# Kernel tuning notes

Hardware: AMD Instinct MI355X
Metric: run time of the kernel (lower is better)

Reference implementation:

```python
import jax, jax.numpy as jnp
import numpy as np
import math

N_EMBD = 1024
N_HEAD = 16
BLOCK = 2048
B, T = 2, 2048


def setup_inputs() -> dict:
    key = jax.random.key(0)
    ks = jax.random.split(key, 5)
    s = 0.02
    return {
        "x": jax.random.normal(ks[0], (B, T, N_EMBD), dtype=jnp.float32),
        "W_attn": jax.random.normal(ks[1], (3 * N_EMBD, N_EMBD), dtype=jnp.float32) * s,  # [out,in] torch layout
        "b_attn": jax.random.normal(ks[2], (3 * N_EMBD,), dtype=jnp.float32) * s,
        "W_proj": jax.random.normal(ks[3], (N_EMBD, N_EMBD), dtype=jnp.float32) * s,
        "b_proj": jax.random.normal(ks[4], (N_EMBD,), dtype=jnp.float32) * s,
    }


def reference(x, W_attn, b_attn, W_proj, b_proj):
    Bx, Tx, C = x.shape
    H = N_HEAD
    D = C // H
    qkv = jnp.einsum("btc,oc->bto", x, W_attn) + b_attn  # [B,T,3C]
    q, k, v = jnp.split(qkv, 3, axis=-1)
    # [B,T,H,D] -> [B,H,T,D]
    q = q.reshape(Bx, Tx, H, D).transpose(0, 2, 1, 3)
    k = k.reshape(Bx, Tx, H, D).transpose(0, 2, 1, 3)
    v = v.reshape(Bx, Tx, H, D).transpose(0, 2, 1, 3)
    att = jnp.einsum("bhqd,bhkd->bhqk", q, k) * (1.0 / math.sqrt(D))
    causal = jnp.tril(jnp.ones((Tx, Tx), dtype=bool))
    att = jnp.where(causal[None, None], att, -jnp.inf)
    att = jax.nn.softmax(att, axis=-1)
    y = jnp.einsum("bhqk,bhkd->bhqd", att, v)  # [B,H,T,D]
    y = y.transpose(0, 2, 1, 3).reshape(Bx, Tx, C)
    y = jnp.einsum("btc,oc->bto", y, W_proj) + b_proj
    return y
```

## Files before the change

### kernel.cpp

```cpp
#include <hip/hip_runtime.h>
#include <hip/hip_bf16.h>
#include <stdint.h>

typedef unsigned short u16;
using f32x4 = __attribute__((ext_vector_type(4))) float;
using s16x8 = __attribute__((ext_vector_type(8))) short;

#define B_SZ 2
#define T_SZ 2048
#define C_SZ 1024
#define H_SZ 16
#define D_SZ 64

__device__ __forceinline__ u16 f2bf(float f) {
  union { float f; uint32_t u; } c; c.f = f;
  uint32_t u = c.u;
  u += 0x7FFFu + ((u >> 16) & 1u);
  return (u16)(u >> 16);
}

__device__ __forceinline__ void async16(const u16* g, u16* l) {
  __builtin_amdgcn_global_load_lds((__attribute__((address_space(1))) void*)(g),
                                   (__attribute__((address_space(3))) void*)(l),
                                   16, 0, 0);
}

__global__ void cvt3_kernel(const float* __restrict__ a, int na,
                            const float* __restrict__ b, int nb,
                            const float* __restrict__ c, int nc,
                            u16* __restrict__ out) {
  int n = na + nb + nc;
  for (int i = blockIdx.x * blockDim.x + threadIdx.x; i < n; i += gridDim.x * blockDim.x) {
    const float* src; int off;
    if (i < na)           { src = a; off = i; }
    else if (i < na + nb) { src = b; off = i - na; }
    else                  { src = c; off = i - na - nb; }
    float4 v = reinterpret_cast<const float4*>(src)[off];
    ushort4 o;
    o.x = f2bf(v.x); o.y = f2bf(v.y); o.z = f2bf(v.z); o.w = f2bf(v.w);
    reinterpret_cast<ushort4*>(out)[i] = o;
  }
}

__global__ __launch_bounds__(256) void gemm_qkv(
    const u16* __restrict__ A, const u16* __restrict__ W,
    const float* __restrict__ bias,
    u16* __restrict__ Qo, u16* __restrict__ Ko, u16* __restrict__ Vt)
{
  const int K = 1024;
  const int NT = 32;
  __shared__ __align__(16) u16 lA[2][128 * 32];
  __shared__ __align__(16) u16 lB[2][128 * 32];
  int tid = threadIdx.x, lane = tid & 63, wave = tid >> 6;
  int wm = (wave >> 1) * 64, wn = (wave & 1) * 64;
  int bm = blockIdx.x * 128, bn = blockIdx.y * 128;
  int r = lane & 15, g = lane >> 4;

  int p0 = tid, p1 = 256 + tid;
  int ar0 = p0 >> 2, ar1 = p1 >> 2;
  int al0 = (p0 & 3) ^ (ar0 & 3), al1 = (p1 & 3) ^ (ar1 & 3);
  const u16* As0 = A + (size_t)(bm + ar0) * K + al0 * 8;
  const u16* As1 = A + (size_t)(bm + ar1) * K + al1 * 8;
  const u16* Ws0 = W + (size_t)(bn + ar0) * K + al0 * 8;
  const u16* Ws1 = W + (size_t)(bn + ar1) * K + al1 * 8;

  f32x4 acc[4][4];
#pragma unroll
  for (int i = 0; i < 4; ++i)
#pragma unroll
    for (int j = 0; j < 4; ++j)
      acc[i][j] = (f32x4){0.f, 0.f, 0.f, 0.f};

  int rd_off = r * 32 + ((g ^ (r & 3)) * 8);

  async16(As0, &lA[0][p0 * 8]);
  async16(As1, &lA[0][p1 * 8]);
  async16(Ws0, &lB[0][p0 * 8]);
  async16(Ws1, &lB[0][p1 * 8]);
  __syncthreads();

  int cur = 0;
  for (int t = 0; t < NT; ++t) {
    if (t + 1 < NT) {
      int k0 = (t + 1) * 32;
      int nb_ = cur ^ 1;
      async16(As0 + k0, &lA[nb_][p0 * 8]);
      async16(As1 + k0, &lA[nb_][p1 * 8]);
      async16(Ws0 + k0, &lB[nb_][p0 * 8]);
      async16(Ws1 + k0, &lB[nb_][p1 * 8]);
    }
    s16x8 af[4], bf[4];
#pragma unroll
    for (int i = 0; i < 4; ++i)
      af[i] = *(const s16x8*)(&lA[cur][(wm + i * 16) * 32 + rd_off]);
#pragma unroll
    for (int j = 0; j < 4; ++j)
      bf[j] = *(const s16x8*)(&lB[cur][(wn + j * 16) * 32 + rd_off]);
#pragma unroll
    for (int i = 0; i < 4; ++i)
#pragma unroll
      for (int j = 0; j < 4; ++j)
        acc[i][j] = __builtin_amdgcn_mfma_f32_16x16x32_bf16(af[i], bf[j], acc[i][j], 0, 0, 0);
    __syncthreads();
    cur ^= 1;
  }

  int seg = bn >> 10;
#pragma unroll
  for (int i = 0; i < 4; ++i) {
#pragma unroll
    for (int j = 0; j < 4; ++j) {
      int col = bn + wn + j * 16 + r;
      int cc = col & 1023;
      int h = cc >> 6, d = cc & 63;
      float bv = bias[col];
      int row0 = bm + wm + i * 16 + g * 4;
      int b = row0 >> 11, t0 = row0 & 2047;
      if (seg == 2) {
        ushort4 pv;
        pv.x = f2bf(acc[i][j][0] + bv);
        pv.y = f2bf(acc[i][j][1] + bv);
        pv.z = f2bf(acc[i][j][2] + bv);
        pv.w = f2bf(acc[i][j][3] + bv);
        *reinterpret_cast<ushort4*>(Vt + ((size_t)(b * H_SZ + h) * D_SZ + d) * T_SZ + t0) = pv;
      } else {
        u16* dst = (seg == 0) ? Qo : Ko;
        float scale = (seg == 0) ? 0.125f : 1.0f;
#pragma unroll
        for (int rr = 0; rr < 4; ++rr) {
          float v = (acc[i][j][rr] + bv) * scale;
          dst[(((size_t)(b * H_SZ + h) * T_SZ + (t0 + rr)) * D_SZ) + d] = f2bf(v);
        }
      }
    }
  }
}

__global__ __launch_bounds__(256) void gemm_proj(
    const u16* __restrict__ A, const u16* __restrict__ W,
    const float* __restrict__ bias, float* __restrict__ out)
{
  const int K = 1024;
  const int NT = 32;
  __shared__ __align__(16) u16 lA[2][128 * 32];
  __shared__ __align__(16) u16 lB[2][128 * 32];
  int tid = threadIdx.x, lane = tid & 63, wave = tid >> 6;
  int wm = (wave >> 1) * 64, wn = (wave & 1) * 64;
  int bm = blockIdx.x * 128, bn = blockIdx.y * 128;
  int r = lane & 15, g = lane >> 4;

  int p0 = tid, p1 = 256 + tid;
  int ar0 = p0 >> 2, ar1 = p1 >> 2;
  int al0 = (p0 & 3) ^ (ar0 & 3), al1 = (p1 & 3) ^ (ar1 & 3);
  const u16* As0 = A + (size_t)(bm + ar0) * K + al0 * 8;
  const u16* As1 = A + (size_t)(bm + ar1) * K + al1 * 8;
  const u16* Ws0 = W + (size_t)(bn + ar0) * K + al0 * 8;
  const u16* Ws1 = W + (size_t)(bn + ar1) * K + al1 * 8;

  f32x4 acc[4][4];
#pragma unroll
  for (int i = 0; i < 4; ++i)
#pragma unroll
    for (int j = 0; j < 4; ++j)
      acc[i][j] = (f32x4){0.f, 0.f, 0.f, 0.f};

  int rd_off = r * 32 + ((g ^ (r & 3)) * 8);

  async16(As0, &lA[0][p0 * 8]);
  async16(As1, &lA[0][p1 * 8]);
  async16(Ws0, &lB[0][p0 * 8]);
  async16(Ws1, &lB[0][p1 * 8]);
  __syncthreads();

  int cur = 0;
  for (int t = 0; t < NT; ++t) {
    if (t + 1 < NT) {
      int k0 = (t + 1) * 32;
      int nb_ = cur ^ 1;
      async16(As0 + k0, &lA[nb_][p0 * 8]);
      async16(As1 + k0, &lA[nb_][p1 * 8]);
      async16(Ws0 + k0, &lB[nb_][p0 * 8]);
      async16(Ws1 + k0, &lB[nb_][p1 * 8]);
    }
    s16x8 af[4], bf[4];
#pragma unroll
    for (int i = 0; i < 4; ++i)
      af[i] = *(const s16x8*)(&lA[cur][(wm + i * 16) * 32 + rd_off]);
#pragma unroll
    for (int j = 0; j < 4; ++j)
      bf[j] = *(const s16x8*)(&lB[cur][(wn + j * 16) * 32 + rd_off]);
#pragma unroll
    for (int i = 0; i < 4; ++i)
#pragma unroll
      for (int j = 0; j < 4; ++j)
        acc[i][j] = __builtin_amdgcn_mfma_f32_16x16x32_bf16(af[i], bf[j], acc[i][j], 0, 0, 0);
    __syncthreads();
    cur ^= 1;
  }

#pragma unroll
  for (int i = 0; i < 4; ++i) {
#pragma unroll
    for (int j = 0; j < 4; ++j) {
      int col = bn + wn + j * 16 + r;
      float bv = bias[col];
#pragma unroll
      for (int rr = 0; rr < 4; ++rr) {
        int row = bm + wm + i * 16 + g * 4 + rr;
        out[(size_t)row * 1024 + col] = acc[i][j][rr] + bv;
      }
    }
  }
}

__global__ __launch_bounds__(256) void attn_kernel(
    const u16* __restrict__ Q, const u16* __restrict__ K, const u16* __restrict__ Vt,
    u16* __restrict__ Y)
{
  __shared__ __align__(16) u16 lK[2][64 * 64];
  __shared__ __align__(16) u16 lV[2][64 * 64];
  __shared__ __align__(16) u16 lP[4][16 * 64];
  int tid = threadIdx.x, lane = tid & 63, wave = tid >> 6;
  int bh = blockIdx.x;
  int qt = 31 - blockIdx.y;
  const u16* Qh = Q + (size_t)bh * T_SZ * D_SZ;
  const u16* Kh = K + (size_t)bh * T_SZ * D_SZ;
  const u16* Vh = Vt + (size_t)bh * D_SZ * T_SZ;
  int r = lane & 15, g = lane >> 4;
  int wq = qt * 64 + wave * 16;
  int qrow = wq + r;

  s16x8 qf0 = *(const s16x8*)(Qh + (size_t)qrow * 64 + g * 8);
  s16x8 qf1 = *(const s16x8*)(Qh + (size_t)qrow * 64 + 32 + g * 8);

  int p0 = tid, p1 = 256 + tid;
  int r0 = p0 >> 3, r1 = p1 >> 3;
  int l0 = (p0 & 7) ^ (r0 & 7), l1 = (p1 & 7) ^ (r1 & 7);

  float m = -3e30f, s = 0.f;
  f32x4 o[4];
#pragma unroll
  for (int j = 0; j < 4; ++j) o[j] = (f32x4){0.f, 0.f, 0.f, 0.f};

  u16* lPw = lP[wave];

  async16(Kh + (size_t)r0 * 64 + l0 * 8, &lK[0][p0 * 8]);
  async16(Kh + (size_t)r1 * 64 + l1 * 8, &lK[0][p1 * 8]);
  async16(Vh + (size_t)r0 * T_SZ + l0 * 8, &lV[0][p0 * 8]);
  async16(Vh + (size_t)r1 * T_SZ + l1 * 8, &lV[0][p1 * 8]);
  __syncthreads();

  int cur = 0;
  for (int kt = 0; kt <= qt; ++kt) {
    int kvbase = kt * 64;
    if (kt < qt) {
      int nb_ = cur ^ 1;
      int kb = kvbase + 64;
      async16(Kh + (size_t)(kb + r0) * 64 + l0 * 8, &lK[nb_][p0 * 8]);
      async16(Kh + (size_t)(kb + r1) * 64 + l1 * 8, &lK[nb_][p1 * 8]);
      async16(Vh + (size_t)r0 * T_SZ + kb + l0 * 8, &lV[nb_][p0 * 8]);
      async16(Vh + (size_t)r1 * T_SZ + kb + l1 * 8, &lV[nb_][p1 * 8]);
    }

    f32x4 sf[4];
#pragma unroll
    for (int jj = 0; jj < 4; ++jj) {
      int krow = jj * 16 + r;
      const s16x8 kf0 = *(const s16x8*)(&lK[cur][krow * 64 + ((g ^ (r & 7)) * 8)]);
      const s16x8 kf1 = *(const s16x8*)(&lK[cur][krow * 64 + (((4 + g) ^ (r & 7)) * 8)]);
      f32x4 sv = (f32x4){0.f, 0.f, 0.f, 0.f};
      sv = __builtin_amdgcn_mfma_f32_16x16x32_bf16(kf0, qf0, sv, 0, 0, 0);
      sv = __builtin_amdgcn_mfma_f32_16x16x32_bf16(kf1, qf1, sv, 0, 0, 0);
      sf[jj] = sv;
    }

    float mx = -3e30f;
    if (kt == qt) {
#pragma unroll
      for (int jj = 0; jj < 4; ++jj)
#pragma unroll
        for (int rr = 0; rr < 4; ++rr) {
          int kv = kvbase + jj * 16 + g * 4 + rr;
          float v = (kv <= qrow) ? sf[jj][rr] : -3e30f;
          sf[jj][rr] = v;
          mx = fmaxf(mx, v);
        }
    } else {
#pragma unroll
      for (int jj = 0; jj < 4; ++jj)
#pragma unroll
        for (int rr = 0; rr < 4; ++rr) mx = fmaxf(mx, sf[jj][rr]);
    }
    mx = fmaxf(mx, __shfl_xor(mx, 16));
    mx = fmaxf(mx, __shfl_xor(mx, 32));

    float mnew = fmaxf(m, mx);
    float corr = __expf(m - mnew);
    m = mnew;

    float rsum = 0.f;
#pragma unroll
    for (int jj = 0; jj < 4; ++jj)
#pragma unroll
      for (int rr = 0; rr < 4; ++rr) {
        float p = __expf(sf[jj][rr] - m);
        sf[jj][rr] = p;
        rsum += p;
      }
    rsum += __shfl_xor(rsum, 16);
    rsum += __shfl_xor(rsum, 32);
    s = s * corr + rsum;

    float crr[4];
#pragma unroll
    for (int rr = 0; rr < 4; ++rr)
      crr[rr] = __shfl(corr, (lane & 48) | (g * 4 + rr), 64);
#pragma unroll
    for (int j = 0; j < 4; ++j)
#pragma unroll
      for (int rr = 0; rr < 4; ++rr) o[j][rr] *= crr[rr];

#pragma unroll
    for (int jj = 0; jj < 4; ++jj) {
      ushort4 pk;
      pk.x = f2bf(sf[jj][0]); pk.y = f2bf(sf[jj][1]);
      pk.z = f2bf(sf[jj][2]); pk.w = f2bf(sf[jj][3]);
      int off = r * 64 + ((jj * 16 + 4 * g) ^ ((r & 7) << 3));
      *reinterpret_cast<ushort4*>(lPw + off) = pk;
    }

#pragma unroll
    for (int hh = 0; hh < 2; ++hh) {
      const s16x8 pa = *(const s16x8*)(lPw + r * 64 + (((hh * 4 + g) ^ (r & 7)) * 8));
#pragma unroll
      for (int j = 0; j < 4; ++j) {
        int vrow = j * 16 + r;
        const s16x8 vb = *(const s16x8*)(&lV[cur][vrow * 64 + (((hh * 4 + g) ^ (r & 7)) * 8)]);
        o[j] = __builtin_amdgcn_mfma_f32_16x16x32_bf16(pa, vb, o[j], 0, 0, 0);
      }
    }
    __syncthreads();
    cur ^= 1;
  }

  float sinv = 1.0f / s;
  float srr[4];
#pragma unroll
  for (int rr = 0; rr < 4; ++rr)
    srr[rr] = __shfl(sinv, (lane & 48) | (g * 4 + rr), 64);

  int b = bh >> 4, h = bh & 15;
#pragma unroll
  for (int j = 0; j < 4; ++j)
#pragma unroll
    for (int rr = 0; rr < 4; ++rr) {
      float v = o[j][rr] * srr[rr];
      int q = wq + g * 4 + rr;
      int d = j * 16 + r;
      Y[((size_t)(b * T_SZ + q)) * C_SZ + h * 64 + d] = f2bf(v);
    }
}

extern "C" void kernel_launch(void* const* d_in, const int* in_sizes, int n_in,
                              void* d_out, int out_size, void* d_ws, size_t ws_size,
                              hipStream_t stream) {
  const float* x      = (const float*)d_in[0];
  const float* W_attn = (const float*)d_in[1];
  const float* b_attn = (const float*)d_in[2];
  const float* W_proj = (const float*)d_in[3];
  const float* b_proj = (const float*)d_in[4];
  float* out = (float*)d_out;

  char* ws = (char*)d_ws;
  u16* xb  = (u16*)ws; ws += (size_t)4096 * 1024 * 2;
  u16* wab = (u16*)ws; ws += (size_t)3072 * 1024 * 2;
  u16* wpb = (u16*)ws; ws += (size_t)1024 * 1024 * 2;
  u16* Qb  = (u16*)ws; ws += (size_t)B_SZ * H_SZ * T_SZ * D_SZ * 2;
  u16* Kb  = (u16*)ws; ws += (size_t)B_SZ * H_SZ * T_SZ * D_SZ * 2;
  u16* Vtb = (u16*)ws; ws += (size_t)B_SZ * H_SZ * T_SZ * D_SZ * 2;
  u16* Yb  = (u16*)ws; ws += (size_t)4096 * 1024 * 2;

  int n4x = 4096 * 1024 / 4;
  int n4a = 3072 * 1024 / 4;
  int n4p = 1024 * 1024 / 4;
  cvt3_kernel<<<2048, 256, 0, stream>>>(x, n4x, W_attn, n4a, W_proj, n4p, xb);

  gemm_qkv<<<dim3(32, 24), 256, 0, stream>>>(xb, wab, b_attn, Qb, Kb, Vtb);
  attn_kernel<<<dim3(32, 32), 256, 0, stream>>>(Qb, Kb, Vtb, Yb);
  gemm_proj<<<dim3(32, 8), 256, 0, stream>>>(Yb, wpb, b_proj, out);
}
```

Before: 121.3 us.

## Use exp2 softmax with lazy rescaling, transposed PV MFMA, and wave priority hints

Folds log2(e) into the Q scale so softmax can use the native exp2 instruction. The running-max rescale of the output accumulator is skipped unless some lane's max grows by more than a threshold. Swapping the MFMA operands in the PV product puts each output row in the lane that owns its softmax state, which removes the cross-lane shuffles for the correction and normalisation factors and allows packed 8-byte output stores. It also raises wave priority around the MFMA blocks and replaces the hand-written bf16 rounding with the library conversion. The lazy rescale lets exponentials reach up to 2^8 before a correction is applied, which slightly changes numerics.

Result: no change. 119.2 us (-1.7%).

```diff
diff --git a/kernel.cpp b/kernel.cpp
--- a/kernel.cpp
+++ b/kernel.cpp
@@ -12,11 +12,11 @@
 #define H_SZ 16
 #define D_SZ 64
 
+#define Q_SCALE 0.18033688011112042f
+
 __device__ __forceinline__ u16 f2bf(float f) {
-  union { float f; uint32_t u; } c; c.f = f;
-  uint32_t u = c.u;
-  u += 0x7FFFu + ((u >> 16) & 1u);
-  return (u16)(u >> 16);
+  __hip_bfloat16 h = __float2bfloat16(f);
+  return *(u16*)&h;
 }
 
 __device__ __forceinline__ void async16(const u16* g, u16* l) {
@@ -125,7 +125,7 @@
         *reinterpret_cast<ushort4*>(Vt + ((size_t)(b * H_SZ + h) * D_SZ + d) * T_SZ + t0) = pv;
       } else {
         u16* dst = (seg == 0) ? Qo : Ko;
-        float scale = (seg == 0) ? 0.125f : 1.0f;
+        float scale = (seg == 0) ? Q_SCALE : 1.0f;
 #pragma unroll
         for (int rr = 0; rr < 4; ++rr) {
           float v = (acc[i][j][rr] + bv) * scale;
@@ -263,6 +263,7 @@
     }
 
     f32x4 sf[4];
+    __builtin_amdgcn_s_setprio(1);
 #pragma unroll
     for (int jj = 0; jj < 4; ++jj) {
       int krow = jj * 16 + r;
@@ -273,6 +274,7 @@
       sv = __builtin_amdgcn_mfma_f32_16x16x32_bf16(kf1, qf1, sv, 0, 0, 0);
       sf[jj] = sv;
     }
+    __builtin_amdgcn_s_setprio(0);
 
     float mx = -3e30f;
     if (kt == qt) {
@@ -294,16 +296,23 @@
     mx = fmaxf(mx, __shfl_xor(mx, 16));
     mx = fmaxf(mx, __shfl_xor(mx, 32));
 
-    float mnew = fmaxf(m, mx);
-    float corr = __expf(m - mnew);
-    m = mnew;
+    float corr = 1.0f;
+    if (!__all(mx <= m + 8.0f)) {
+      float mnew = fmaxf(m, mx);
+      corr = __builtin_amdgcn_exp2f(m - mnew);
+      m = mnew;
+#pragma unroll
+      for (int j = 0; j < 4; ++j)
+#pragma unroll
+        for (int rr = 0; rr < 4; ++rr) o[j][rr] *= corr;
+    }
 
     float rsum = 0.f;
 #pragma unroll
     for (int jj = 0; jj < 4; ++jj)
 #pragma unroll
       for (int rr = 0; rr < 4; ++rr) {
-        float p = __expf(sf[jj][rr] - m);
+        float p = __builtin_amdgcn_exp2f(sf[jj][rr] - m);
         sf[jj][rr] = p;
         rsum += p;
       }
@@ -311,15 +320,6 @@
     rsum += __shfl_xor(rsum, 32);
     s = s * corr + rsum;
 
-    float crr[4];
-#pragma unroll
-    for (int rr = 0; rr < 4; ++rr)
-      crr[rr] = __shfl(corr, (lane & 48) | (g * 4 + rr), 64);
-#pragma unroll
-    for (int j = 0; j < 4; ++j)
-#pragma unroll
-      for (int rr = 0; rr < 4; ++rr) o[j][rr] *= crr[rr];
-
 #pragma unroll
     for (int jj = 0; jj < 4; ++jj) {
       ushort4 pk;
@@ -329,6 +329,7 @@
       *reinterpret_cast<ushort4*>(lPw + off) = pk;
     }
 
+    __builtin_amdgcn_s_setprio(1);
 #pragma unroll
     for (int hh = 0; hh < 2; ++hh) {
       const s16x8 pa = *(const s16x8*)(lPw + r * 64 + (((hh * 4 + g) ^ (r & 7)) * 8));
@@ -336,29 +337,26 @@
       for (int j = 0; j < 4; ++j) {
         int vrow = j * 16 + r;
         const s16x8 vb = *(const s16x8*)(&lV[cur][vrow * 64 + (((hh * 4 + g) ^ (r & 7)) * 8)]);
-        o[j] = __builtin_amdgcn_mfma_f32_16x16x32_bf16(pa, vb, o[j], 0, 0, 0);
+        o[j] = __builtin_amdgcn_mfma_f32_16x16x32_bf16(vb, pa, o[j], 0, 0, 0);
       }
     }
+    __builtin_amdgcn_s_setprio(0);
     __syncthreads();
     cur ^= 1;
   }
 
   float sinv = 1.0f / s;
-  float srr[4];
-#pragma unroll
-  for (int rr = 0; rr < 4; ++rr)
-    srr[rr] = __shfl(sinv, (lane & 48) | (g * 4 + rr), 64);
-
   int b = bh >> 4, h = bh & 15;
-#pragma unroll
-  for (int j = 0; j < 4; ++j)
-#pragma unroll
-    for (int rr = 0; rr < 4; ++rr) {
-      float v = o[j][rr] * srr[rr];
-      int q = wq + g * 4 + rr;
-      int d = j * 16 + r;
-      Y[((size_t)(b * T_SZ + q)) * C_SZ + h * 64 + d] = f2bf(v);
-    }
+  size_t ybase = ((size_t)(b * T_SZ + qrow)) * C_SZ + h * 64;
+#pragma unroll
+  for (int j = 0; j < 4; ++j) {
+    ushort4 pk;
+    pk.x = f2bf(o[j][0] * sinv);
+    pk.y = f2bf(o[j][1] * sinv);
+    pk.z = f2bf(o[j][2] * sinv);
+    pk.w = f2bf(o[j][3] * sinv);
+    *reinterpret_cast<ushort4*>(Y + ybase + j * 16 + g * 4) = pk;
+  }
 }
 
 extern "C" void kernel_launch(void* const* d_in, const int* in_sizes, int n_in,
```
